# Kernel optimization log

Hardware: AMD Instinct MI355X
Metric: run time of the kernel (lower is better)

The kernel has to match this reference:

```python
import jax, jax.numpy as jnp
import numpy as np

# CDF 9/7 (JPEG2000 irreversible) analysis filters
H0 = np.array([0.026748757410810, -0.016864118442875, -0.078223266528990,
               0.266864118442875, 0.602949018236360, 0.266864118442875,
               -0.078223266528990, -0.016864118442875, 0.026748757410810], np.float32)
H1 = np.array([0.091271763114250, -0.057543526228500, -0.591271763114250,
               1.115087052457000, -0.591271763114250, -0.057543526228500,
               0.091271763114250], np.float32)


def conv2d(x, w, stride=(1, 1), padding='VALID', groups=1):
    return jax.lax.conv_general_dilated(
        x, w, stride, padding,
        dimension_numbers=('NCHW', 'OIHW', 'NCHW'),
        feature_group_count=groups)


def partial_spectral_conv(x, mask, weight, bias, u):
    # spectral normalization (one power iteration with fixed u buffer)
    O = weight.shape[0]
    wm = weight.reshape(O, -1)
    v = wm.T @ u
    v = v / (jnp.linalg.norm(v) + 1e-12)
    sigma = jnp.linalg.norm(wm @ v)
    w_sn = weight / sigma
    # partial convolution (NVIDIA-style mask renormalization)
    kh, kw = weight.shape[2], weight.shape[3]
    out = conv2d(x * mask, w_sn, padding=((1, 1), (1, 1)))           # [B,O,H,W]
    msum = conv2d(mask, jnp.ones((1, 1, kh, kw), x.dtype), padding=((1, 1), (1, 1)))
    valid = msum > 0
    ratio = jnp.where(valid, (kh * kw) / jnp.maximum(msum, 1e-8), 0.0)
    out = jnp.where(valid, out * ratio + bias[None, :, None, None], 0.0)
    return out, valid.astype(x.dtype)                                # mask stays [B,1,H,W]


def partial_gdn(x, mask, beta, gamma):
    # divisive normalization: y = x / sqrt(beta + gamma @ x^2), masked
    denom = jnp.sqrt(beta[None, :, None, None] + jnp.einsum('oc,bchw->bohw', gamma, x * x))
    return (x / denom) * mask, mask


def filt(x, f, axis):
    # grouped 1D filter along H (axis=2) or W (axis=3), reflect pad, stride 2
    K = f.shape[0]
    p = (K - 1) // 2
    pads = [(0, 0)] * 4
    pads[axis] = (p, p)
    xp = jnp.pad(x, pads, mode='reflect')
    C = x.shape[1]
    if axis == 2:
        kern = jnp.broadcast_to(f.reshape(1, 1, K, 1), (C, 1, K, 1))
        stride = (2, 1)
    else:
        kern = jnp.broadcast_to(f.reshape(1, 1, 1, K), (C, 1, 1, K))
        stride = (1, 2)
    return conv2d(xp, kern, stride, 'VALID', groups=C)


def mask_down(m, K, axis):
    # mask is valid where any contributing pixel is valid
    cnt = filt(m, jnp.ones((K,), m.dtype), axis)
    return (cnt > 0).astype(m.dtype)


def dwt2d(x, mask):
    h0 = jnp.asarray(H0)
    h1 = jnp.asarray(H1)
    lo_r, hi_r = filt(x, h0, 2), filt(x, h1, 2)
    ll, lh = filt(lo_r, h0, 3), filt(lo_r, h1, 3)
    hl, hh = filt(hi_r, h0, 3), filt(hi_r, h1, 3)
    m_lo, m_hi = mask_down(mask, 9, 2), mask_down(mask, 7, 2)
    m_ll, m_lh = mask_down(m_lo, 9, 3), mask_down(m_lo, 7, 3)
    m_hl, m_hh = mask_down(m_hi, 9, 3), mask_down(m_hi, 7, 3)
    return (ll, lh, hl, hh), (m_ll, m_lh, m_hl, m_hh)


def setup_inputs() -> dict:
    key = jax.random.key(0)
    ks = jax.random.split(key, 6)
    B, Cin, Cout, H, W = 8, 64, 128, 256, 256
    tensor = jax.random.normal(ks[0], (B, Cin, H, W), jnp.float32)
    mask = (jax.random.uniform(ks[1], (B, 1, H, W)) > 0.2).astype(jnp.float32)
    weight = jax.random.normal(ks[2], (Cout, Cin, 3, 3), jnp.float32) * 0.05
    bias = jnp.zeros((Cout,), jnp.float32)
    u = jax.random.normal(ks[3], (Cout,), jnp.float32)
    u = u / jnp.linalg.norm(u)
    beta = jnp.ones((Cout,), jnp.float32)
    gamma = 0.1 * jnp.eye(Cout, dtype=jnp.float32) + 1e-3
    return {"tensor": tensor, "mask": mask, "weight": weight, "bias": bias,
            "u": u, "beta": beta, "gamma": gamma}


def reference(tensor, mask, weight, bias, u, beta, gamma):
    x, m = partial_spectral_conv(tensor, mask, weight, bias, u)
    x, m = partial_gdn(x, m, beta, gamma)
    (ll, lh, hl, hh), (m_ll, m_lh, m_hl, m_hh) = dwt2d(x, m)
    return (ll, m_ll, lh, hl, hh, m_lh, m_hl, m_hh)
```

## Files before the change

### kernel.cpp

```cpp
#include <hip/hip_runtime.h>

#define B 8
#define CIN 64
#define COUT 128
#define H 256
#define W 256
#define HW 65536
#define OH 128
#define OW 128

typedef __attribute__((ext_vector_type(8))) short bf16x8;
typedef __attribute__((ext_vector_type(16))) float f32x16;
typedef __attribute__((ext_vector_type(4))) float f32x4;
typedef __attribute__((ext_vector_type(2))) float f32x2;

__constant__ float c_h0[9] = {0.026748757410810f, -0.016864118442875f, -0.078223266528990f,
                              0.266864118442875f, 0.602949018236360f, 0.266864118442875f,
                              -0.078223266528990f, -0.016864118442875f, 0.026748757410810f};
__constant__ float c_h1[7] = {0.091271763114250f, -0.057543526228500f, -0.591271763114250f,
                              1.115087052457000f, -0.591271763114250f, -0.057543526228500f,
                              0.091271763114250f};

__device__ __forceinline__ unsigned short f2bf(float f) {
    unsigned int x = __float_as_uint(f);
    unsigned int r = (x + 0x7fffu + ((x >> 16) & 1u)) >> 16;
    return (unsigned short)r;
}
__device__ __forceinline__ float bf2f(unsigned short h) {
    return __uint_as_float(((unsigned int)h) << 16);
}
__device__ __forceinline__ int refl(int i) {
    if (i < 0) return -i;
    if (i > 255) return 510 - i;
    return i;
}

__global__ void sigma_kernel(const float* __restrict__ w, const float* __restrict__ u,
                             float* __restrict__ inv_sigma) {
    __shared__ float v[576];
    __shared__ float red[256];
    const int tid = threadIdx.x;
    for (int j = tid; j < 576; j += 256) {
        float s = 0.f;
        for (int o = 0; o < 128; ++o) s += w[o * 576 + j] * u[o];
        v[j] = s;
    }
    __syncthreads();
    float s = 0.f;
    for (int j = tid; j < 576; j += 256) s += v[j] * v[j];
    red[tid] = s;
    __syncthreads();
    for (int off = 128; off > 0; off >>= 1) {
        if (tid < off) red[tid] += red[tid + off];
        __syncthreads();
    }
    const float vn = sqrtf(red[0]) + 1e-12f;
    __syncthreads();
    float tacc = 0.f;
    if (tid < 128) {
        float d = 0.f;
        for (int j = 0; j < 576; ++j) d += w[tid * 576 + j] * v[j];
        d /= vn;
        tacc = d * d;
    }
    red[tid] = tacc;
    __syncthreads();
    for (int off = 128; off > 0; off >>= 1) {
        if (tid < off) red[tid] += red[tid + off];
        __syncthreads();
    }
    if (tid == 0) inv_sigma[0] = 1.f / sqrtf(red[0]);
}

__global__ void prep_kernel(const float* __restrict__ w, const float* __restrict__ gamma,
                            const float* __restrict__ inv_sigma,
                            unsigned short* __restrict__ wt_bf,
                            unsigned short* __restrict__ gamma_bf) {
    const int i = blockIdx.x * 256 + threadIdx.x;
    const float is = inv_sigma[0];
    if (i < 73728) {
        const int o = i / 576, rem = i - o * 576;
        const int c = rem / 9, tap = rem - c * 9;
        wt_bf[(o * 9 + tap) * 64 + c] = f2bf(w[i] * is);
    } else if (i < 90112) {
        const int j = i - 73728;
        gamma_bf[j] = f2bf(gamma[j]);
    }
}

__global__ __launch_bounds__(256, 3) void convgdn_kernel(
    const float* __restrict__ x, const float* __restrict__ mask,
    const unsigned short* __restrict__ wt_bf, const float* __restrict__ bias,
    const unsigned short* __restrict__ gamma_bf, const float* __restrict__ beta,
    unsigned short* __restrict__ t, float* __restrict__ valid) {
    __shared__ __align__(16) char lds[36144];
    unsigned short* raw  = (unsigned short*)lds;
    unsigned short* y2   = (unsigned short*)lds;
    unsigned short* ygdn = (unsigned short*)lds;
    float* mlds = (float*)(lds + 34816);
    float* rlds = (float*)(lds + 35632);

    const int tid = threadIdx.x;
    const int lane = tid & 63;
    const int lo = lane & 31;
    const int hi = lane >> 5;
    const int n0 = (tid >> 6) << 5;
    const int oc = n0 + lo;
    const int b = blockIdx.z;
    const int h0 = blockIdx.y << 2;
    const int wc0 = blockIdx.x << 5;

    if (tid < 204) {
        const int r = tid / 34, cl = tid - r * 34;
        const int hr = h0 - 1 + r, wc = wc0 - 1 + cl;
        float mv = 0.f;
        if (hr >= 0 && hr < H && wc >= 0 && wc < W) mv = mask[b * HW + hr * W + wc];
        mlds[tid] = mv;
    }
    __syncthreads();

    const bool intr = (h0 != 0) && (h0 != 252) && (wc0 != 0) && (wc0 != 224);
    if (intr) {
        const float* xb = x + b * CIN * HW + (h0 - 1) * W + (wc0 - 1);
        for (unsigned i = tid; i < 13056u; i += 256u) {
            const unsigned c = i / 204u, rem = i - c * 204u;
            const unsigned r = rem / 34u, cl = rem - r * 34u;
            const float v = xb[c * HW + r * W + cl] * mlds[rem];
            raw[((r * 8u + (c >> 3)) * 34u + cl) * 8u + (c & 7u)] = f2bf(v);
        }
    } else {
        for (unsigned i = tid; i < 13056u; i += 256u) {
            const unsigned c = i / 204u, rem = i - c * 204u;
            const unsigned r = rem / 34u, cl = rem - r * 34u;
            const int hr = h0 - 1 + (int)r, wc = wc0 - 1 + (int)cl;
            float v = 0.f;
            if (hr >= 0 && hr < H && wc >= 0 && wc < W)
                v = x[((b * CIN + (int)c) * H + hr) * W + wc] * mlds[rem];
            raw[((r * 8u + (c >> 3)) * 34u + cl) * 8u + (c & 7u)] = f2bf(v);
        }
    }
    if (tid < 128) {
        const int mt = tid >> 5, cl = tid & 31;
        float ms = 0.f;
#pragma unroll
        for (int a = 0; a < 3; ++a)
#pragma unroll
            for (int bb = 0; bb < 3; ++bb) ms += mlds[(mt + a) * 34 + cl + bb];
        const bool vld = ms > 0.f;
        rlds[tid] = vld ? 9.f / fmaxf(ms, 1e-8f) : 0.f;
        valid[b * HW + (h0 + mt) * W + wc0 + cl] = vld ? 1.f : 0.f;
    }
    __syncthreads();

    f32x16 acc[4];
#pragma unroll
    for (int mt = 0; mt < 4; ++mt)
#pragma unroll
        for (int r = 0; r < 16; ++r) acc[mt][r] = 0.f;

    for (int kh = 0; kh < 3; ++kh) {
#pragma unroll
        for (int kw = 0; kw < 3; ++kw) {
            const int tap = kh * 3 + kw;
            bf16x8 bw[4];
#pragma unroll
            for (int cc = 0; cc < 4; ++cc)
                bw[cc] = *(const bf16x8*)&wt_bf[(oc * 9 + tap) * 64 + cc * 16 + hi * 8];
#pragma unroll
            for (int cc = 0; cc < 4; ++cc) {
                const int c0 = cc * 16 + hi * 8;
#pragma unroll
                for (int mt = 0; mt < 4; ++mt) {
                    const bf16x8 afrag =
                        *(const bf16x8*)&raw[(((mt + kh) * 8 + (c0 >> 3)) * 34 + (lo + kw)) * 8];
                    acc[mt] = __builtin_amdgcn_mfma_f32_32x32x16_bf16(afrag, bw[cc], acc[mt], 0, 0, 0);
                }
            }
        }
    }
    __syncthreads();

    const float bs = bias[oc];
    const float bt = beta[oc];
#pragma unroll
    for (int mt = 0; mt < 4; ++mt) {
#pragma unroll
        for (int r = 0; r < 16; ++r) {
            const int rowq = (r & 3) + 8 * (r >> 2) + 4 * hi;
            const float rat = rlds[mt * 32 + rowq];
            const float y = (rat > 0.f) ? acc[mt][r] * rat + bs : 0.f;
            acc[mt][r] = y;
            y2[(mt * 32 + rowq) * 136 + oc] = f2bf(y * y);
        }
    }
    __syncthreads();

    f32x16 acc2[4];
#pragma unroll
    for (int g = 0; g < 4; ++g)
#pragma unroll
        for (int r = 0; r < 16; ++r) acc2[g][r] = 0.f;

    for (int ch = 0; ch < 8; ++ch) {
        const int c0 = ch * 16 + hi * 8;
        const bf16x8 gb = *(const bf16x8*)&gamma_bf[oc * 128 + c0];
#pragma unroll
        for (int g = 0; g < 4; ++g) {
            const bf16x8 ga = *(const bf16x8*)&y2[(g * 32 + lo) * 136 + c0];
            acc2[g] = __builtin_amdgcn_mfma_f32_32x32x16_bf16(ga, gb, acc2[g], 0, 0, 0);
        }
    }
    __syncthreads();

#pragma unroll
    for (int mt = 0; mt < 4; ++mt) {
#pragma unroll
        for (int rg = 0; rg < 4; ++rg) {
            const int base = 8 * rg + 4 * hi;
            ushort4 pk;
            unsigned short* pp = (unsigned short*)&pk;
#pragma unroll
            for (int j = 0; j < 4; ++j) {
                const int r = rg * 4 + j;
                const float d = bt + acc2[mt][r];
                pp[j] = f2bf(acc[mt][r] * rsqrtf(d));
            }
            *(ushort4*)&ygdn[oc * 132 + mt * 32 + base] = pk;
        }
    }
    __syncthreads();

#pragma unroll
    for (int it = 0; it < 2; ++it) {
        const int idx = it * 256 + tid;
        const int oc2 = idx >> 2, mt2 = idx & 3;
        const unsigned short* src = &ygdn[oc2 * 132 + mt2 * 32];
        unsigned short* dst = &t[((b * COUT + oc2) * H + h0 + mt2) * W + wc0];
#pragma unroll
        for (int k = 0; k < 8; ++k)
            *(ushort4*)(dst + k * 4) = *(const ushort4*)(src + k * 4);
    }
}

__global__ void dwt_kernel(const unsigned short* __restrict__ y, float* __restrict__ out) {
    __shared__ float ys[40][76];
    __shared__ float lof[16][76];
    __shared__ float hif[16][76];
    const int tid = threadIdx.x;
    const int wt_ = blockIdx.x & 3;
    const int ht_ = blockIdx.x >> 2;
    const int bc = blockIdx.y;
    const int ho0 = ht_ * 16, wo0 = wt_ * 32;
    const int r0 = 2 * ho0 - 4, c0 = 2 * wo0 - 4;
    const unsigned short* yb = y + bc * HW;

    for (unsigned i = tid; i < 720u; i += 256u) {
        const int lr = (int)(i / 18u);
        const int ch4 = (int)(i - (unsigned)lr * 18u) << 2;
        const int gr = refl(r0 + lr);
        const int col = c0 + ch4;
        const int colc = col < 0 ? 0 : (col > 252 ? 252 : col);
        const ushort4 v = *(const ushort4*)(yb + gr * W + colc);
        if (col == colc) {
            f32x4 f;
            f.x = bf2f(v.x); f.y = bf2f(v.y); f.z = bf2f(v.z); f.w = bf2f(v.w);
            *(f32x4*)&ys[lr][ch4] = f;
        }
    }
    if (wt_ == 0) {
        for (int i = tid; i < 160; i += 256) {
            const int lr = i >> 2, q = i & 3;
            ys[lr][q] = bf2f(yb[refl(r0 + lr) * W + (4 - q)]);
        }
    } else if (wt_ == 3) {
        for (int i = tid; i < 160; i += 256) {
            const int lr = i >> 2, q = i & 3;
            ys[lr][68 + q] = bf2f(yb[refl(r0 + lr) * W + (254 - q)]);
        }
    }
    __syncthreads();

    for (unsigned i = tid; i < 288u; i += 256u) {
        const int r = (int)(i / 18u);
        const int ch4 = (int)(i - (unsigned)r * 18u) << 2;
        f32x4 vv[9];
#pragma unroll
        for (int k = 0; k < 9; ++k) vv[k] = *(const f32x4*)&ys[2 * r + k][ch4];
        f32x4 sl = c_h0[0] * vv[0];
#pragma unroll
        for (int k = 1; k < 9; ++k) sl += c_h0[k] * vv[k];
        f32x4 sh = c_h1[0] * vv[1];
#pragma unroll
        for (int k = 1; k < 7; ++k) sh += c_h1[k] * vv[k + 1];
        *(f32x4*)&lof[r][ch4] = sl;
        *(f32x4*)&hif[r][ch4] = sh;
    }
    __syncthreads();

    const int rr = tid >> 4;
    const int q = tid & 15;
    const f32x4 a0 = *(const f32x4*)&lof[rr][4 * q];
    const f32x4 a1 = *(const f32x4*)&lof[rr][4 * q + 4];
    const f32x4 a2 = *(const f32x4*)&lof[rr][4 * q + 8];
    const f32x4 b0 = *(const f32x4*)&hif[rr][4 * q];
    const f32x4 b1 = *(const f32x4*)&hif[rr][4 * q + 4];
    const f32x4 b2 = *(const f32x4*)&hif[rr][4 * q + 8];
    float L[12], M[12];
#pragma unroll
    for (int m = 0; m < 4; ++m) {
        L[m] = a0[m]; L[m + 4] = a1[m]; L[m + 8] = a2[m];
        M[m] = b0[m]; M[m + 4] = b1[m]; M[m + 8] = b2[m];
    }
    float ll0 = 0.f, ll1 = 0.f, hl0 = 0.f, hl1 = 0.f;
#pragma unroll
    for (int k = 0; k < 9; ++k) {
        ll0 += c_h0[k] * L[k];
        ll1 += c_h0[k] * L[k + 2];
        hl0 += c_h0[k] * M[k];
        hl1 += c_h0[k] * M[k + 2];
    }
    float lh0 = 0.f, lh1 = 0.f, hh0 = 0.f, hh1 = 0.f;
#pragma unroll
    for (int k = 0; k < 7; ++k) {
        lh0 += c_h1[k] * L[k + 1];
        lh1 += c_h1[k] * L[k + 3];
        hh0 += c_h1[k] * M[k + 1];
        hh1 += c_h1[k] * M[k + 3];
    }
    const int idx = (bc * OH + ho0 + rr) * OW + wo0 + 2 * q;
    f32x2 s;
    s.x = ll0; s.y = ll1; *(f32x2*)&out[idx] = s;
    s.x = lh0; s.y = lh1; *(f32x2*)&out[16908288 + idx] = s;
    s.x = hl0; s.y = hl1; *(f32x2*)&out[33685504 + idx] = s;
    s.x = hh0; s.y = hh1; *(f32x2*)&out[50462720 + idx] = s;
}

__global__ void dwtmask_kernel(const float* __restrict__ valid, float* __restrict__ out) {
    const int g = blockIdx.x * 256 + threadIdx.x;
    const int b = g >> 14;
    const int rem = g & 16383;
    const int i = rem >> 7, j = rem & 127;
    const float* vb = valid + b * HW;
    bool bll = false, blh = false, bhl = false, bhh = false;
    for (int k1 = 0; k1 < 9; ++k1) {
        const int rr = refl(2 * i - 4 + k1);
        const bool in7r = (k1 >= 1 && k1 <= 7);
        for (int k2 = 0; k2 < 9; ++k2) {
            const int cc = refl(2 * j - 4 + k2);
            if (vb[rr * W + cc] > 0.f) {
                const bool in7c = (k2 >= 1 && k2 <= 7);
                bll = true;
                blh |= in7c;
                bhl |= in7r;
                bhh |= (in7r && in7c);
            }
        }
    }
    out[16777216 + g] = bll ? 1.f : 0.f;
    out[67239936 + g] = blh ? 1.f : 0.f;
    out[67371008 + g] = bhl ? 1.f : 0.f;
    out[67502080 + g] = bhh ? 1.f : 0.f;
}

extern "C" void kernel_launch(void* const* d_in, const int* in_sizes, int n_in,
                              void* d_out, int out_size, void* d_ws, size_t ws_size,
                              hipStream_t stream) {
    const float* x     = (const float*)d_in[0];
    const float* mask  = (const float*)d_in[1];
    const float* w     = (const float*)d_in[2];
    const float* bias  = (const float*)d_in[3];
    const float* u     = (const float*)d_in[4];
    const float* beta  = (const float*)d_in[5];
    const float* gamma = (const float*)d_in[6];
    float* out = (float*)d_out;

    float* f_ws = (float*)d_ws;
    float* inv_sigma = f_ws;
    unsigned short* wt_bf    = (unsigned short*)(f_ws + 256);
    unsigned short* gamma_bf = wt_bf + 73728;
    float* valid = (float*)(gamma_bf + 16384);
    unsigned short* t = (unsigned short*)(valid + 524288);

    sigma_kernel<<<1, 256, 0, stream>>>(w, u, inv_sigma);
    prep_kernel<<<352, 256, 0, stream>>>(w, gamma, inv_sigma, wt_bf, gamma_bf);
    convgdn_kernel<<<dim3(8, 64, 8), 256, 0, stream>>>(x, mask, wt_bf, bias, gamma_bf, beta,
                                                       t, valid);
    dwt_kernel<<<dim3(32, 1024), 256, 0, stream>>>(t, out);
    dwtmask_kernel<<<512, 256, 0, stream>>>(valid, out);
}
```

Before: 717.2 us.

## Vectorize conv staging, swizzle LDS, remap block order, widen sigma kernel

Several independent changes. The sigma kernel now runs with 1024 threads and splits the row dot products across 8 threads each. The conv input staging loads float4 pairs of channels and writes packed bf16 pairs, instead of doing scalar loads. The y^2 and GDN output LDS buffers use XOR swizzles, and the GDN matmul is done one m-tile at a time to cut accumulator registers. Blocks in both the conv and DWT kernels are remapped in an XCD-interleaved order, and the DWT loads are batched before being converted. Together these aim to reduce global load instructions, LDS bank conflicts and register pressure, at the cost of extra syncs and more complex indexing.

Result: faster. 673.5 us (-6.1%).

```diff
diff --git a/kernel.cpp b/kernel.cpp
--- a/kernel.cpp
+++ b/kernel.cpp
@@ -38,38 +38,45 @@
 __global__ void sigma_kernel(const float* __restrict__ w, const float* __restrict__ u,
                              float* __restrict__ inv_sigma) {
     __shared__ float v[576];
-    __shared__ float red[256];
+    __shared__ float red[1024];
+    __shared__ float d2[128];
     const int tid = threadIdx.x;
-    for (int j = tid; j < 576; j += 256) {
+    if (tid < 576) {
         float s = 0.f;
-        for (int o = 0; o < 128; ++o) s += w[o * 576 + j] * u[o];
-        v[j] = s;
-    }
-    __syncthreads();
-    float s = 0.f;
-    for (int j = tid; j < 576; j += 256) s += v[j] * v[j];
-    red[tid] = s;
-    __syncthreads();
-    for (int off = 128; off > 0; off >>= 1) {
+        for (int o = 0; o < 128; ++o) s += w[o * 576 + tid] * u[o];
+        v[tid] = s;
+    }
+    __syncthreads();
+    red[tid] = (tid < 576) ? v[tid] * v[tid] : 0.f;
+    __syncthreads();
+    for (int off = 512; off > 0; off >>= 1) {
         if (tid < off) red[tid] += red[tid + off];
         __syncthreads();
     }
     const float vn = sqrtf(red[0]) + 1e-12f;
     __syncthreads();
-    float tacc = 0.f;
+    const int o = tid >> 3, p = tid & 7;
+    const float* wr = w + o * 576 + p * 72;
+    const float* vv = v + p * 72;
+    float part = 0.f;
+    for (int j = 0; j < 72; j += 4) {
+        const f32x4 wv = *(const f32x4*)(wr + j);
+        part += wv.x * vv[j] + wv.y * vv[j + 1] + wv.z * vv[j + 2] + wv.w * vv[j + 3];
+    }
+    red[tid] = part;
+    __syncthreads();
     if (tid < 128) {
         float d = 0.f;
-        for (int j = 0; j < 576; ++j) d += w[tid * 576 + j] * v[j];
+        for (int k = 0; k < 8; ++k) d += red[tid * 8 + k];
         d /= vn;
-        tacc = d * d;
-    }
-    red[tid] = tacc;
-    __syncthreads();
-    for (int off = 128; off > 0; off >>= 1) {
-        if (tid < off) red[tid] += red[tid + off];
+        d2[tid] = d * d;
+    }
+    __syncthreads();
+    for (int off = 64; off > 0; off >>= 1) {
+        if (tid < off) d2[tid] += d2[tid + off];
         __syncthreads();
     }
-    if (tid == 0) inv_sigma[0] = 1.f / sqrtf(red[0]);
+    if (tid == 0) inv_sigma[0] = 1.f / sqrtf(d2[0]);
 }
 
 __global__ void prep_kernel(const float* __restrict__ w, const float* __restrict__ gamma,
@@ -93,12 +100,11 @@
     const unsigned short* __restrict__ wt_bf, const float* __restrict__ bias,
     const unsigned short* __restrict__ gamma_bf, const float* __restrict__ beta,
     unsigned short* __restrict__ t, float* __restrict__ valid) {
-    __shared__ __align__(16) char lds[36144];
-    unsigned short* raw  = (unsigned short*)lds;
-    unsigned short* y2   = (unsigned short*)lds;
-    unsigned short* ygdn = (unsigned short*)lds;
-    float* mlds = (float*)(lds + 34816);
-    float* rlds = (float*)(lds + 35632);
+    __shared__ __align__(16) char lds[38192];
+    unsigned short* raw = (unsigned short*)lds;
+    unsigned short* y2  = (unsigned short*)lds;
+    float* mlds = (float*)(lds + 36864);
+    float* rlds = (float*)(lds + 37680);
 
     const int tid = threadIdx.x;
     const int lane = tid & 63;
@@ -106,9 +112,12 @@
     const int hi = lane >> 5;
     const int n0 = (tid >> 6) << 5;
     const int oc = n0 + lo;
-    const int b = blockIdx.z;
-    const int h0 = blockIdx.y << 2;
-    const int wc0 = blockIdx.x << 5;
+    const int bid = blockIdx.x;
+    const int work = ((bid & 7) << 9) | (bid >> 3);
+    const int b = work >> 9;
+    const int rem0 = work & 511;
+    const int h0 = (rem0 >> 3) << 2;
+    const int wc0 = (rem0 & 7) << 5;
 
     if (tid < 204) {
         const int r = tid / 34, cl = tid - r * 34;
@@ -121,12 +130,27 @@
 
     const bool intr = (h0 != 0) && (h0 != 252) && (wc0 != 0) && (wc0 != 224);
     if (intr) {
-        const float* xb = x + b * CIN * HW + (h0 - 1) * W + (wc0 - 1);
-        for (unsigned i = tid; i < 13056u; i += 256u) {
-            const unsigned c = i / 204u, rem = i - c * 204u;
-            const unsigned r = rem / 34u, cl = rem - r * 34u;
-            const float v = xb[c * HW + r * W + cl] * mlds[rem];
-            raw[((r * 8u + (c >> 3)) * 34u + cl) * 8u + (c & 7u)] = f2bf(v);
+        const float* xb = x + ((size_t)b * CIN) * HW + (h0 - 1) * W + (wc0 - 4);
+        for (unsigned i = tid; i < 1920u; i += 256u) {
+            const unsigned q = i % 10u;
+            const unsigned rc = i / 10u;
+            const unsigned r = rc % 6u;
+            const unsigned cp = rc / 6u;
+            const float* p0 = xb + (2u * cp) * HW + r * W + 4u * q;
+            const f32x4 va = *(const f32x4*)p0;
+            const f32x4 vb2 = *(const f32x4*)(p0 + HW);
+            unsigned short* base = &raw[((r * 8u + (cp >> 2)) * 34u) * 8u + 2u * (cp & 3u)];
+            const float* mrow = &mlds[r * 34u];
+#pragma unroll
+            for (int k = 0; k < 4; ++k) {
+                const int cl = 4 * (int)q - 3 + k;
+                if ((unsigned)cl <= 33u) {
+                    const float mv = mrow[cl];
+                    const unsigned int pk = (unsigned int)f2bf(va[k] * mv) |
+                                            ((unsigned int)f2bf(vb2[k] * mv) << 16);
+                    *(unsigned int*)(base + (unsigned)cl * 8u) = pk;
+                }
+            }
         }
     } else {
         for (unsigned i = tid; i < 13056u; i += 256u) {
@@ -190,42 +214,39 @@
             const float rat = rlds[mt * 32 + rowq];
             const float y = (rat > 0.f) ? acc[mt][r] * rat + bs : 0.f;
             acc[mt][r] = y;
-            y2[(mt * 32 + rowq) * 136 + oc] = f2bf(y * y);
-        }
-    }
-    __syncthreads();
-
-    f32x16 acc2[4];
-#pragma unroll
-    for (int g = 0; g < 4; ++g)
-#pragma unroll
-        for (int r = 0; r < 16; ++r) acc2[g][r] = 0.f;
-
-    for (int ch = 0; ch < 8; ++ch) {
-        const int c0 = ch * 16 + hi * 8;
-        const bf16x8 gb = *(const bf16x8*)&gamma_bf[oc * 128 + c0];
-#pragma unroll
-        for (int g = 0; g < 4; ++g) {
-            const bf16x8 ga = *(const bf16x8*)&y2[(g * 32 + lo) * 136 + c0];
-            acc2[g] = __builtin_amdgcn_mfma_f32_32x32x16_bf16(ga, gb, acc2[g], 0, 0, 0);
+            y2[(mt * 32 + rowq) * 144 + (oc ^ ((rowq & 7) << 3))] = f2bf(y * y);
         }
     }
     __syncthreads();
 
 #pragma unroll
     for (int mt = 0; mt < 4; ++mt) {
+        f32x16 a2;
+#pragma unroll
+        for (int r = 0; r < 16; ++r) a2[r] = 0.f;
+        const int row = mt * 32 + lo;
+        const int swz = (lo & 7) << 3;
+#pragma unroll
+        for (int ch = 0; ch < 8; ++ch) {
+            const int c0 = ch * 16 + hi * 8;
+            const bf16x8 gb = *(const bf16x8*)&gamma_bf[oc * 128 + c0];
+            const bf16x8 ga = *(const bf16x8*)&y2[row * 144 + (c0 ^ swz)];
+            a2 = __builtin_amdgcn_mfma_f32_32x32x16_bf16(ga, gb, a2, 0, 0, 0);
+        }
+        __syncthreads();
+        unsigned short* yg = (unsigned short*)lds + mt * 4608;
 #pragma unroll
         for (int rg = 0; rg < 4; ++rg) {
-            const int base = 8 * rg + 4 * hi;
             ushort4 pk;
             unsigned short* pp = (unsigned short*)&pk;
 #pragma unroll
             for (int j = 0; j < 4; ++j) {
                 const int r = rg * 4 + j;
-                const float d = bt + acc2[mt][r];
+                const float d = bt + a2[r];
                 pp[j] = f2bf(acc[mt][r] * rsqrtf(d));
             }
-            *(ushort4*)&ygdn[oc * 132 + mt * 32 + base] = pk;
+            const int pxc = 2 * rg + hi;
+            *(ushort4*)&yg[oc * 36 + ((pxc ^ (oc & 7)) << 2)] = pk;
         }
     }
     __syncthreads();
@@ -233,12 +254,13 @@
 #pragma unroll
     for (int it = 0; it < 2; ++it) {
         const int idx = it * 256 + tid;
-        const int oc2 = idx >> 2, mt2 = idx & 3;
-        const unsigned short* src = &ygdn[oc2 * 132 + mt2 * 32];
+        const int oc2 = idx & 127, mt2 = idx >> 7;
+        const unsigned short* src = (const unsigned short*)lds + mt2 * 4608 + oc2 * 36;
         unsigned short* dst = &t[((b * COUT + oc2) * H + h0 + mt2) * W + wc0];
+        const int s7 = oc2 & 7;
 #pragma unroll
         for (int k = 0; k < 8; ++k)
-            *(ushort4*)(dst + k * 4) = *(const ushort4*)(src + k * 4);
+            *(ushort4*)(dst + k * 4) = *(const ushort4*)(src + ((k ^ s7) << 2));
     }
 }
 
@@ -247,24 +269,38 @@
     __shared__ float lof[16][76];
     __shared__ float hif[16][76];
     const int tid = threadIdx.x;
-    const int wt_ = blockIdx.x & 3;
-    const int ht_ = blockIdx.x >> 2;
-    const int bc = blockIdx.y;
+    const int bid = blockIdx.x;
+    const int work = ((bid & 7) << 12) | (bid >> 3);
+    const int bc = work >> 5;
+    const int tile = work & 31;
+    const int wt_ = tile & 3;
+    const int ht_ = tile >> 2;
     const int ho0 = ht_ * 16, wo0 = wt_ * 32;
     const int r0 = 2 * ho0 - 4, c0 = 2 * wo0 - 4;
     const unsigned short* yb = y + bc * HW;
 
-    for (unsigned i = tid; i < 720u; i += 256u) {
-        const int lr = (int)(i / 18u);
-        const int ch4 = (int)(i - (unsigned)lr * 18u) << 2;
-        const int gr = refl(r0 + lr);
-        const int col = c0 + ch4;
-        const int colc = col < 0 ? 0 : (col > 252 ? 252 : col);
-        const ushort4 v = *(const ushort4*)(yb + gr * W + colc);
-        if (col == colc) {
+    ushort4 va[3];
+    int ldst[3];
+#pragma unroll
+    for (int k = 0; k < 3; ++k) {
+        const int i = tid + (k << 8);
+        ldst[k] = -1;
+        if (i < 720) {
+            const int lr = i / 18;
+            const int ch4 = (i - lr * 18) << 2;
+            const int col = c0 + ch4;
+            if ((unsigned)col <= 252u) {
+                va[k] = *(const ushort4*)(yb + refl(r0 + lr) * W + col);
+                ldst[k] = lr * 76 + ch4;
+            }
+        }
+    }
+#pragma unroll
+    for (int k = 0; k < 3; ++k) {
+        if (ldst[k] >= 0) {
             f32x4 f;
-            f.x = bf2f(v.x); f.y = bf2f(v.y); f.z = bf2f(v.z); f.w = bf2f(v.w);
-            *(f32x4*)&ys[lr][ch4] = f;
+            f.x = bf2f(va[k].x); f.y = bf2f(va[k].y); f.z = bf2f(va[k].z); f.w = bf2f(va[k].w);
+            *(f32x4*)&((float*)ys)[ldst[k]] = f;
         }
     }
     if (wt_ == 0) {
@@ -381,10 +417,9 @@
     float* valid = (float*)(gamma_bf + 16384);
     unsigned short* t = (unsigned short*)(valid + 524288);
 
-    sigma_kernel<<<1, 256, 0, stream>>>(w, u, inv_sigma);
+    sigma_kernel<<<1, 1024, 0, stream>>>(w, u, inv_sigma);
     prep_kernel<<<352, 256, 0, stream>>>(w, gamma, inv_sigma, wt_bf, gamma_bf);
-    convgdn_kernel<<<dim3(8, 64, 8), 256, 0, stream>>>(x, mask, wt_bf, bias, gamma_bf, beta,
-                                                       t, valid);
-    dwt_kernel<<<dim3(32, 1024), 256, 0, stream>>>(t, out);
+    convgdn_kernel<<<4096, 256, 0, stream>>>(x, mask, wt_bf, bias, gamma_bf, beta, t, valid);
+    dwt_kernel<<<32768, 256, 0, stream>>>(t, out);
     dwtmask_kernel<<<512, 256, 0, stream>>>(valid, out);
 }
```
